# Performance work log

Hardware: AMD Instinct MI355X
Metric: run time of the kernel (lower is better)

The kernel has to match this reference:

```python
import jax, jax.numpy as jnp
import numpy as np

MARGIN = 1.0
B, C, D = 16384, 1000, 128


def setup_inputs() -> dict:
    key = jax.random.key(0)
    k1, k2, k3 = jax.random.split(key, 3)
    features = jax.random.normal(k1, (B, D), dtype=jnp.float32)
    targets = jax.random.randint(k2, (B,), 0, C, dtype=jnp.int64)
    class_feature_vectors = jax.random.normal(k3, (C, D), dtype=jnp.float32)
    return {"features": features, "targets": targets,
            "class_feature_vectors": class_feature_vectors}


def reference(features, targets, class_feature_vectors):
    # Squared L2 distance between every sample and every class vector:
    # dist[i, j] = sum_d (features[i, d] - class_vecs[j, d])^2
    # computed via the expansion ||f||^2 + ||c||^2 - 2 f.c to avoid a [B, C, D]
    # intermediate.
    f2 = jnp.sum(features * features, axis=1)                      # [B]
    c2 = jnp.sum(class_feature_vectors * class_feature_vectors, axis=1)  # [C]
    cross = jnp.einsum('bd,cd->bc', features, class_feature_vectors)     # [B, C]
    dist = f2[:, None] + c2[None, :] - 2.0 * cross                 # [B, C]
    # Hinge term for every NEGATIVE class (j != target[i]).
    hinge = jax.nn.relu(MARGIN - dist)                             # [B, C]
    neg_mask = targets[:, None] != jnp.arange(dist.shape[1])[None, :]
    loss = jnp.sum(jnp.where(neg_mask, hinge, 0.0)) / dist.shape[0]
    return loss
```

## Files before the change

kernel.cpp:

```cpp
#include <hip/hip_runtime.h>
#include <stdint.h>

#define B_N 16384
#define C_N 1000
#define D_N 128
#define MARGIN 1.0f
#define NBLK 1024

typedef __attribute__((ext_vector_type(8))) short short8;
typedef __attribute__((ext_vector_type(4))) float f32x4;

__device__ __forceinline__ short f2bf(float f) {
    union { float f; uint32_t u; } v; v.f = f;
    uint32_t u = v.u;
    return (short)((u + 0x7FFFu + ((u >> 16) & 1u)) >> 16);
}

__device__ __forceinline__ short8 cvt8(const float4& v0, const float4& v1) {
    short8 s;
    s[0] = f2bf(v0.x); s[1] = f2bf(v0.y); s[2] = f2bf(v0.z); s[3] = f2bf(v0.w);
    s[4] = f2bf(v1.x); s[5] = f2bf(v1.y); s[6] = f2bf(v1.z); s[7] = f2bf(v1.w);
    return s;
}

__device__ __forceinline__ void load_bfrag(const short* __restrict__ bpre,
                                           int nb, int lane, short8* dst) {
    const short8* bp = reinterpret_cast<const short8*>(bpre + (size_t)nb * 2048) + lane;
    dst[0] = bp[0];
    dst[1] = bp[64];
    dst[2] = bp[128];
    dst[3] = bp[192];
}

__global__ __launch_bounds__(64) void prep_kernel(
    const float* __restrict__ cls, short* __restrict__ bpre,
    float* __restrict__ c2p)
{
    const int nb   = blockIdx.x;
    const int lane = threadIdx.x;
    const int l15  = lane & 15;
    const int kg   = lane >> 4;
    const int col  = nb * 16 + l15;
    const bool valid = col < C_N;

    float sq = 0.f;
    #pragma unroll
    for (int kk = 0; kk < 4; ++kk) {
        float4 v0 = make_float4(0.f, 0.f, 0.f, 0.f);
        float4 v1 = make_float4(0.f, 0.f, 0.f, 0.f);
        if (valid) {
            const float* p = cls + (size_t)col * D_N + kk * 32 + kg * 8;
            v0 = *reinterpret_cast<const float4*>(p);
            v1 = *reinterpret_cast<const float4*>(p + 4);
        }
        sq += v0.x*v0.x + v0.y*v0.y + v0.z*v0.z + v0.w*v0.w
            + v1.x*v1.x + v1.y*v1.y + v1.z*v1.z + v1.w*v1.w;
        *reinterpret_cast<short8*>(bpre + (size_t)(nb * 2048 + kk * 512 + lane * 8))
            = cvt8(v0, v1);
    }
    sq += __shfl_xor(sq, 16);
    sq += __shfl_xor(sq, 32);
    if (lane < 16)
        c2p[nb * 16 + lane] = ((nb * 16 + lane) < C_N) ? sq : 1e30f;
}

__global__ __launch_bounds__(256, 4) void closs_kernel(
    const float* __restrict__ feat, const long long* __restrict__ tgt,
    const short* __restrict__ bpre, const float* __restrict__ c2p,
    float* __restrict__ part)
{
    const int tid  = threadIdx.x;
    const int wave = tid >> 6;
    const int lane = tid & 63;
    const int l15  = lane & 15;
    const int kg   = lane >> 4;

    const int bid  = blockIdx.x;
    const int xcd  = bid & 7;
    const int idx  = bid >> 3;
    const int by   = (xcd << 5) | (idx >> 2);
    const int bx   = idx & 3;
    const int row0 = by * 64 + wave * 16;
    const int nb0  = bx * 16;

    short8 b0[4], b1[4];
    load_bfrag(bpre, nb0 + 0, lane, b0);
    load_bfrag(bpre, nb0 + 1, lane, b1);

    float c2r[16];
    #pragma unroll
    for (int i = 0; i < 16; ++i) c2r[i] = c2p[(nb0 + i) * 16 + l15];

    short8 a[4];
    float sq = 0.f;
    const float* ap = feat + (size_t)(row0 + l15) * D_N + kg * 8;
    #pragma unroll
    for (int kk = 0; kk < 4; ++kk) {
        float4 v0 = *reinterpret_cast<const float4*>(ap + kk * 32);
        float4 v1 = *reinterpret_cast<const float4*>(ap + kk * 32 + 4);
        sq += v0.x*v0.x + v0.y*v0.y + v0.z*v0.z + v0.w*v0.w
            + v1.x*v1.x + v1.y*v1.y + v1.z*v1.z + v1.w*v1.w;
        a[kk] = cvt8(v0, v1);
    }
    sq += __shfl_xor(sq, 16);
    sq += __shfl_xor(sq, 32);
    float t[4]; int tg[4];
    #pragma unroll
    for (int r = 0; r < 4; ++r) {
        t[r]  = MARGIN - __shfl(sq, kg * 4 + r);
        tg[r] = (int)tgt[row0 + kg * 4 + r];
    }

    float hsum = 0.f;
    #pragma unroll
    for (int i = 0; i < 16; ++i) {
        short8* bc = (i & 1) ? b1 : b0;
        f32x4 pA = (f32x4){0.f, 0.f, 0.f, 0.f};
        f32x4 pB = (f32x4){0.f, 0.f, 0.f, 0.f};
        pA = __builtin_amdgcn_mfma_f32_16x16x32_bf16(a[0], bc[0], pA, 0, 0, 0);
        pB = __builtin_amdgcn_mfma_f32_16x16x32_bf16(a[1], bc[1], pB, 0, 0, 0);
        pA = __builtin_amdgcn_mfma_f32_16x16x32_bf16(a[2], bc[2], pA, 0, 0, 0);
        pB = __builtin_amdgcn_mfma_f32_16x16x32_bf16(a[3], bc[3], pB, 0, 0, 0);
        if (i + 2 < 16)
            load_bfrag(bpre, nb0 + i + 2, lane, bc);

        const float c2v = c2r[i];
        float u[4];
        #pragma unroll
        for (int r = 0; r < 4; ++r)
            u[r] = __builtin_fmaf(2.0f, pA[r] + pB[r], t[r] - c2v);
        const float mx = fmaxf(fmaxf(u[0], u[1]), fmaxf(u[2], u[3]));
        if (__any(mx > 0.0f)) {
            const int col = (nb0 + i) * 16 + l15;
            #pragma unroll
            for (int r = 0; r < 4; ++r)
                hsum += (col != tg[r]) ? fmaxf(0.0f, u[r]) : 0.0f;
        }
    }

    #pragma unroll
    for (int off = 32; off; off >>= 1) hsum += __shfl_down(hsum, off);
    __shared__ float ws[4];
    if (lane == 0) ws[wave] = hsum;
    __syncthreads();
    if (tid == 0)
        part[bid] = ws[0] + ws[1] + ws[2] + ws[3];
}

__global__ __launch_bounds__(256) void reduce_kernel(
    const float* __restrict__ part, float* __restrict__ out)
{
    const int tid = threadIdx.x;
    float s = part[tid] + part[tid + 256] + part[tid + 512] + part[tid + 768];
    #pragma unroll
    for (int off = 32; off; off >>= 1) s += __shfl_down(s, off);
    __shared__ float ws[4];
    if ((tid & 63) == 0) ws[tid >> 6] = s;
    __syncthreads();
    if (tid == 0) out[0] = (ws[0] + ws[1] + ws[2] + ws[3]) * (1.0f / 16384.0f);
}

extern "C" void kernel_launch(void* const* d_in, const int* in_sizes, int n_in,
                              void* d_out, int out_size, void* d_ws, size_t ws_size,
                              hipStream_t stream) {
    const float*     feat = (const float*)d_in[0];
    const long long* tgt  = (const long long*)d_in[1];
    const float*     cls  = (const float*)d_in[2];
    float*           out  = (float*)d_out;

    short* bpre = (short*)d_ws;
    float* c2p  = (float*)((char*)d_ws + 64 * 2048 * sizeof(short));
    float* part = c2p + 1024;

    prep_kernel<<<64, 64, 0, stream>>>(cls, bpre, c2p);
    closs_kernel<<<NBLK, 256, 0, stream>>>(feat, tgt, bpre, c2p, part);
    reduce_kernel<<<1, 256, 0, stream>>>(part, out);
}
```

Measured before the change: 24.30 us.

## Reshape wave tile to 32 rows by 8 column-blocks to reuse B fragments

```diff
diff --git a/kernel.cpp b/kernel.cpp
--- a/kernel.cpp
+++ b/kernel.cpp
@@ -78,63 +78,76 @@
     const int bid  = blockIdx.x;
     const int xcd  = bid & 7;
     const int idx  = bid >> 3;
-    const int by   = (xcd << 5) | (idx >> 2);
-    const int bx   = idx & 3;
-    const int row0 = by * 64 + wave * 16;
-    const int nb0  = bx * 16;
+    const int by   = (xcd << 4) | (idx >> 3);
+    const int bx   = idx & 7;
+    const int row0 = by * 128 + wave * 32;
+    const int nb0  = bx * 8;
 
     short8 b0[4], b1[4];
     load_bfrag(bpre, nb0 + 0, lane, b0);
     load_bfrag(bpre, nb0 + 1, lane, b1);
 
-    float c2r[16];
+    float c2r[8];
     #pragma unroll
-    for (int i = 0; i < 16; ++i) c2r[i] = c2p[(nb0 + i) * 16 + l15];
+    for (int i = 0; i < 8; ++i) c2r[i] = c2p[(nb0 + i) * 16 + l15];
 
-    short8 a[4];
-    float sq = 0.f;
-    const float* ap = feat + (size_t)(row0 + l15) * D_N + kg * 8;
+    short8 a[2][4];
+    float  t[2][4];
+    int    tg[2][4];
     #pragma unroll
-    for (int kk = 0; kk < 4; ++kk) {
-        float4 v0 = *reinterpret_cast<const float4*>(ap + kk * 32);
-        float4 v1 = *reinterpret_cast<const float4*>(ap + kk * 32 + 4);
-        sq += v0.x*v0.x + v0.y*v0.y + v0.z*v0.z + v0.w*v0.w
-            + v1.x*v1.x + v1.y*v1.y + v1.z*v1.z + v1.w*v1.w;
-        a[kk] = cvt8(v0, v1);
-    }
-    sq += __shfl_xor(sq, 16);
-    sq += __shfl_xor(sq, 32);
-    float t[4]; int tg[4];
-    #pragma unroll
-    for (int r = 0; r < 4; ++r) {
-        t[r]  = MARGIN - __shfl(sq, kg * 4 + r);
-        tg[r] = (int)tgt[row0 + kg * 4 + r];
+    for (int rg = 0; rg < 2; ++rg) {
+        const float* ap = feat + (size_t)(row0 + rg * 16 + l15) * D_N + kg * 8;
+        float s = 0.f;
+        #pragma unroll
+        for (int kk = 0; kk < 4; ++kk) {
+            float4 v0 = *reinterpret_cast<const float4*>(ap + kk * 32);
+            float4 v1 = *reinterpret_cast<const float4*>(ap + kk * 32 + 4);
+            s += v0.x*v0.x + v0.y*v0.y + v0.z*v0.z + v0.w*v0.w
+               + v1.x*v1.x + v1.y*v1.y + v1.z*v1.z + v1.w*v1.w;
+            a[rg][kk] = cvt8(v0, v1);
+        }
+        s += __shfl_xor(s, 16);
+        s += __shfl_xor(s, 32);
+        #pragma unroll
+        for (int r = 0; r < 4; ++r) {
+            t[rg][r]  = MARGIN - __shfl(s, kg * 4 + r);
+            tg[rg][r] = (int)tgt[row0 + rg * 16 + kg * 4 + r];
+        }
     }
 
     float hsum = 0.f;
     #pragma unroll
-    for (int i = 0; i < 16; ++i) {
+    for (int i = 0; i < 8; ++i) {
         short8* bc = (i & 1) ? b1 : b0;
-        f32x4 pA = (f32x4){0.f, 0.f, 0.f, 0.f};
-        f32x4 pB = (f32x4){0.f, 0.f, 0.f, 0.f};
-        pA = __builtin_amdgcn_mfma_f32_16x16x32_bf16(a[0], bc[0], pA, 0, 0, 0);
-        pB = __builtin_amdgcn_mfma_f32_16x16x32_bf16(a[1], bc[1], pB, 0, 0, 0);
-        pA = __builtin_amdgcn_mfma_f32_16x16x32_bf16(a[2], bc[2], pA, 0, 0, 0);
-        pB = __builtin_amdgcn_mfma_f32_16x16x32_bf16(a[3], bc[3], pB, 0, 0, 0);
-        if (i + 2 < 16)
+        f32x4 p0 = (f32x4){0.f, 0.f, 0.f, 0.f};
+        f32x4 p1 = (f32x4){0.f, 0.f, 0.f, 0.f};
+        p0 = __builtin_amdgcn_mfma_f32_16x16x32_bf16(a[0][0], bc[0], p0, 0, 0, 0);
+        p1 = __builtin_amdgcn_mfma_f32_16x16x32_bf16(a[1][0], bc[0], p1, 0, 0, 0);
+        p0 = __builtin_amdgcn_mfma_f32_16x16x32_bf16(a[0][1], bc[1], p0, 0, 0, 0);
+        p1 = __builtin_amdgcn_mfma_f32_16x16x32_bf16(a[1][1], bc[1], p1, 0, 0, 0);
+        p0 = __builtin_amdgcn_mfma_f32_16x16x32_bf16(a[0][2], bc[2], p0, 0, 0, 0);
+        p1 = __builtin_amdgcn_mfma_f32_16x16x32_bf16(a[1][2], bc[2], p1, 0, 0, 0);
+        p0 = __builtin_amdgcn_mfma_f32_16x16x32_bf16(a[0][3], bc[3], p0, 0, 0, 0);
+        p1 = __builtin_amdgcn_mfma_f32_16x16x32_bf16(a[1][3], bc[3], p1, 0, 0, 0);
+        if (i + 2 < 8)
             load_bfrag(bpre, nb0 + i + 2, lane, bc);
 
         const float c2v = c2r[i];
-        float u[4];
+        float u0[4], u1[4];
         #pragma unroll
-        for (int r = 0; r < 4; ++r)
-            u[r] = __builtin_fmaf(2.0f, pA[r] + pB[r], t[r] - c2v);
-        const float mx = fmaxf(fmaxf(u[0], u[1]), fmaxf(u[2], u[3]));
+        for (int r = 0; r < 4; ++r) {
+            u0[r] = __builtin_fmaf(2.0f, p0[r], t[0][r] - c2v);
+            u1[r] = __builtin_fmaf(2.0f, p1[r], t[1][r] - c2v);
+        }
+        const float mx = fmaxf(fmaxf(fmaxf(u0[0], u0[1]), fmaxf(u0[2], u0[3])),
+                               fmaxf(fmaxf(u1[0], u1[1]), fmaxf(u1[2], u1[3])));
         if (__any(mx > 0.0f)) {
             const int col = (nb0 + i) * 16 + l15;
             #pragma unroll
-            for (int r = 0; r < 4; ++r)
-                hsum += (col != tg[r]) ? fmaxf(0.0f, u[r]) : 0.0f;
+            for (int r = 0; r < 4; ++r) {
+                hsum += (col != tg[0][r]) ? fmaxf(0.0f, u0[r]) : 0.0f;
+                hsum += (col != tg[1][r]) ? fmaxf(0.0f, u1[r]) : 0.0f;
+            }
         }
     }
 
```

Result: slower. 27.34 us (+12.5%).
